# Kernel optimization log

Hardware: AMD Instinct MI355X
Metric: run time of the kernel (lower is better)

Reference implementation:

```python
import jax, jax.numpy as jnp
import numpy as np

N = 40000
E = 640000
IN_FEATS = 128
OUT_FEATS = 64
K = 8
FACTOR_DIM = OUT_FEATS // K  # 8
ITERATIONS = 3
TAU = 1.0
LEAKY_SLOPE = 0.01  # torch nn.LeakyReLU default


def setup_inputs() -> dict:
    key = jax.random.key(0)
    k1, k2, k3 = jax.random.split(key, 3)
    x = jax.random.normal(k1, (N, IN_FEATS), dtype=jnp.float32)
    # xavier_normal_ with gain=1.414: std = gain * sqrt(2 / (fan_in + fan_out))
    std = 1.414 * np.sqrt(2.0 / (IN_FEATS + OUT_FEATS))
    weight = jax.random.normal(k2, (IN_FEATS, OUT_FEATS), dtype=jnp.float32) * std
    bias = jnp.zeros((OUT_FEATS,), dtype=jnp.float32)
    edge_index = jax.random.randint(k3, (2, E), 0, N, dtype=jnp.int32)
    return {"x": x, "weight": weight, "bias": bias, "edge_index": edge_index}


def _l2norm(h):
    # h / ||h||_2 along last dim (no eps, matching torch code)
    return h / jnp.sqrt((h * h).sum(-1, keepdims=True))


def reference(x, weight, bias, edge_index):
    num_nodes = x.shape[0]
    src = edge_index[0]  # scatter target / softmax segment node
    dst = edge_index[1]  # gathered neighbor node

    h = jax.nn.leaky_relu(x @ weight + bias, LEAKY_SLOPE)          # [N, out]
    # split into K factors of FACTOR_DIM: [N, K, d]
    h = h.reshape(num_nodes, K, FACTOR_DIM)
    h_normed = _l2norm(h)                                           # [N, K, d]

    h_src = h_normed
    h_dst = h_normed
    for _ in range(ITERATIONS):
        feat_nbr = h_src[dst]                                       # [E, K, d]
        s = (h_dst[src] * feat_nbr).sum(-1) / TAU                   # [E, K]
        # segment softmax over edges grouped by src node
        smax = jax.ops.segment_max(s, src, num_segments=num_nodes)  # [N, K]
        ex = jnp.exp(s - smax[src])                                 # [E, K]
        denom = jax.ops.segment_sum(ex, src, num_segments=num_nodes)
        alpha = ex / denom[src]                                     # [E, K]
        msg = feat_nbr * alpha[..., None]                           # [E, K, d]
        node_attr = jax.ops.segment_sum(msg, src, num_segments=num_nodes)
        node_attr = node_attr + h_normed                            # [N, K, d]
        h_dst = _l2norm(node_attr)
    return h_dst.reshape(num_nodes, -1)                             # [N, out]
```

## Files before the change

### kernel.cpp

```cpp
#include <hip/hip_runtime.h>
#include <math.h>

#define NN   40000
#define EE   640000
#define INF_ 128
#define OUTF 64
#define SLOTS 64

#define NB32  1250
#define NCOLS 40
#define NBINS (NB32 * NCOLS)
#define SCANA_BLOCKS ((NBINS + 255) / 256)
#define NG4  (EE / 4)

typedef float f2 __attribute__((ext_vector_type(2)));

__device__ __forceinline__ f2 pkfma(f2 a, f2 b, f2 c) {
    return __builtin_elementwise_fma(a, b, c);
}
__device__ __forceinline__ f2 shf2(f2 a, int m) {
    f2 b; b.x = __shfl_xor(a.x, m); b.y = __shfl_xor(a.y, m); return b;
}
__device__ __forceinline__ f2 bfpair(unsigned u) {
    f2 c;
    c.x = __uint_as_float(u << 16);
    c.y = __uint_as_float(u & 0xffff0000u);
    return c;
}
__device__ __forceinline__ unsigned short f2bf(float f) {
    unsigned u = __float_as_uint(f);
    return (unsigned short)((u + 0x7fffu + ((u >> 16) & 1u)) >> 16);
}


__global__ __launch_bounds__(256) void count_gemm_k(
        const float* __restrict__ x, const float* __restrict__ w,
        const float* __restrict__ bias, float* __restrict__ hn,
        unsigned short* __restrict__ hn16,
        const int4* __restrict__ src4, int* __restrict__ binsT,
        uchar4* __restrict__ lrank4) {
    __shared__ float wl[INF_ * OUTF];
    __shared__ float xl[4][8 * 132];

    if (blockIdx.x < NCOLS) {
        int b = blockIdx.x;
        int* lbin = (int*)wl;
        for (int i = threadIdx.x; i < NB32; i += 256) lbin[i] = 0;
        __syncthreads();
#pragma unroll
        for (int rnd = 0; rnd < 16; ++rnd) {
            int gi = b * 4096 + rnd * 256 + threadIdx.x;
            if (gi < NG4) {
                int4 s = src4[gi];
                uchar4 lr;
                lr.x = (unsigned char)atomicAdd(&lbin[s.x >> 5], 1);
                lr.y = (unsigned char)atomicAdd(&lbin[s.y >> 5], 1);
                lr.z = (unsigned char)atomicAdd(&lbin[s.z >> 5], 1);
                lr.w = (unsigned char)atomicAdd(&lbin[s.w >> 5], 1);
                lrank4[gi] = lr;
            }
        }
        __syncthreads();
        for (int u = threadIdx.x; u < NB32; u += 256) binsT[u * NCOLS + b] = lbin[u];
        return;
    }

    for (int i = threadIdx.x; i < INF_ * OUTF; i += 256) wl[i] = w[i];

    int wv = threadIdx.x >> 6;
    int l  = threadIdx.x & 63;
    int q  = l >> 4;
    int rr = l & 15;
    float4 bv = ((const float4*)bias)[rr];
    int srow = l >> 5;
    int scol = (l & 31) * 4;

    int nb = ((blockIdx.x - NCOLS) * 4 + wv) * 16;

#pragma unroll
    for (int h = 0; h < 2; ++h) {
        int n0 = nb + h * 8;
        {
            const float4* xs = (const float4*)(x + (size_t)n0 * INF_);
#pragma unroll
            for (int j = 0; j < 4; ++j) {
                float4 v = xs[j * 64 + l];
                *(float4*)&xl[wv][(j * 2 + srow) * 132 + scol] = v;
            }
        }
        if (h == 0) __syncthreads();
        float4 a0 = bv, a1 = bv;
        const float* x0 = &xl[wv][q * 132];
        const float* x1 = &xl[wv][(q + 4) * 132];
#pragma unroll 4
        for (int i = 0; i < INF_; ++i) {
            float4 w4 = ((const float4*)wl)[i * 16 + rr];
            float xv0 = x0[i], xv1 = x1[i];
            a0.x = fmaf(xv0, w4.x, a0.x); a0.y = fmaf(xv0, w4.y, a0.y);
            a0.z = fmaf(xv0, w4.z, a0.z); a0.w = fmaf(xv0, w4.w, a0.w);
            a1.x = fmaf(xv1, w4.x, a1.x); a1.y = fmaf(xv1, w4.y, a1.y);
            a1.z = fmaf(xv1, w4.z, a1.z); a1.w = fmaf(xv1, w4.w, a1.w);
        }
        a0.x = a0.x > 0.f ? a0.x : 0.01f * a0.x;
        a0.y = a0.y > 0.f ? a0.y : 0.01f * a0.y;
        a0.z = a0.z > 0.f ? a0.z : 0.01f * a0.z;
        a0.w = a0.w > 0.f ? a0.w : 0.01f * a0.w;
        a1.x = a1.x > 0.f ? a1.x : 0.01f * a1.x;
        a1.y = a1.y > 0.f ? a1.y : 0.01f * a1.y;
        a1.z = a1.z > 0.f ? a1.z : 0.01f * a1.z;
        a1.w = a1.w > 0.f ? a1.w : 0.01f * a1.w;
        float s0 = a0.x*a0.x + a0.y*a0.y + a0.z*a0.z + a0.w*a0.w;
        float s1 = a1.x*a1.x + a1.y*a1.y + a1.z*a1.z + a1.w*a1.w;
        s0 += __shfl_xor(s0, 1);
        s1 += __shfl_xor(s1, 1);
        float v0 = rsqrtf(s0), v1 = rsqrtf(s1);
        float4 o0 = make_float4(a0.x*v0, a0.y*v0, a0.z*v0, a0.w*v0);
        float4 o1 = make_float4(a1.x*v1, a1.y*v1, a1.z*v1, a1.w*v1);
        ((float4*)hn)[(size_t)(n0 + q) * 16 + rr] = o0;
        ((float4*)hn)[(size_t)(n0 + 4 + q) * 16 + rr] = o1;
        ushort4 u0, u1;
        u0.x = f2bf(o0.x); u0.y = f2bf(o0.y); u0.z = f2bf(o0.z); u0.w = f2bf(o0.w);
        u1.x = f2bf(o1.x); u1.y = f2bf(o1.y); u1.z = f2bf(o1.z); u1.w = f2bf(o1.w);
        ((ushort4*)hn16)[(size_t)(n0 + q) * 16 + rr] = u0;
        ((ushort4*)hn16)[(size_t)(n0 + 4 + q) * 16 + rr] = u1;
    }
}


__global__ void scanA_k(const int* __restrict__ binsT, int* __restrict__ excl,
                        int* __restrict__ bsum) {
    __shared__ int tmp[256];
    int i = blockIdx.x * 256 + threadIdx.x;
    int v = (i < NBINS) ? binsT[i] : 0;
    tmp[threadIdx.x] = v;
    __syncthreads();
    for (int off = 1; off < 256; off <<= 1) {
        int t = (threadIdx.x >= off) ? tmp[threadIdx.x - off] : 0;
        __syncthreads();
        tmp[threadIdx.x] += t;
        __syncthreads();
    }
    if (i < NBINS) excl[i] = tmp[threadIdx.x] - v;
    if (threadIdx.x == 255) bsum[blockIdx.x] = tmp[255];
}

__device__ __forceinline__ void spine_scan(const int* __restrict__ bsum, int* spine) {
    int v = (threadIdx.x < SCANA_BLOCKS) ? bsum[threadIdx.x] : 0;
    spine[threadIdx.x] = v;
    __syncthreads();
    for (int off = 1; off < 256; off <<= 1) {
        int t = (threadIdx.x >= off) ? spine[threadIdx.x - off] : 0;
        __syncthreads();
        spine[threadIdx.x] += t;
        __syncthreads();
    }
    spine[threadIdx.x] -= v;
    __syncthreads();
}


__global__ __launch_bounds__(256) void part_k(const int4* __restrict__ src4,
                                              const int4* __restrict__ dst4,
                                              const uchar4* __restrict__ lrank4,
                                              const int* __restrict__ excl,
                                              const int* __restrict__ bsum,
                                              unsigned* __restrict__ part) {
    __shared__ int spine[256];
    spine_scan(bsum, spine);

    int gi = blockIdx.x * 256 + threadIdx.x;
    int b  = gi >> 12;
    int4 s = src4[gi];
    int4 d = dst4[gi];
    uchar4 lr = lrank4[gi];
    int i0 = (s.x >> 5) * NCOLS + b;
    int i1 = (s.y >> 5) * NCOLS + b;
    int i2 = (s.z >> 5) * NCOLS + b;
    int i3 = (s.w >> 5) * NCOLS + b;
    part[excl[i0] + spine[i0 >> 8] + lr.x] = ((unsigned)d.x << 5) | (unsigned)(s.x & 31);
    part[excl[i1] + spine[i1 >> 8] + lr.y] = ((unsigned)d.y << 5) | (unsigned)(s.y & 31);
    part[excl[i2] + spine[i2 >> 8] + lr.z] = ((unsigned)d.z << 5) | (unsigned)(s.z & 31);
    part[excl[i3] + spine[i3 >> 8] + lr.w] = ((unsigned)d.w << 5) | (unsigned)(s.w & 31);
}


__global__ __launch_bounds__(256) void attn_build_k(const uint4* __restrict__ hg,
                                                    const float* __restrict__ hnf,
                                                    float* __restrict__ out,
                                                    const unsigned* __restrict__ part,
                                                    const int* __restrict__ excl,
                                                    const int* __restrict__ bsum) {
    __shared__ unsigned short csr_l[32][SLOTS];
    __shared__ int cnt[32];
    __shared__ int spine[256];

    spine_scan(bsum, spine);

    int nb = blockIdx.x;
    if (threadIdx.x < 32) cnt[threadIdx.x] = 0;
    __syncthreads();

    int iu = nb * NCOLS;
    int beg = excl[iu] + spine[iu >> 8];
    int end = EE;
    if (nb + 1 < NB32) {
        int iv = (nb + 1) * NCOLS;
        end = excl[iv] + spine[iv >> 8];
    }
    for (int e = beg + threadIdx.x; e < end; e += 256) {
        unsigned p = part[e];
        int lo = (int)(p & 31u);
        int lr = atomicAdd(&cnt[lo], 1);
        if (lr < SLOTS) csr_l[lo][lr] = (unsigned short)(p >> 5);
    }
    __syncthreads();

    int wv = threadIdx.x >> 6;
    int l  = threadIdx.x & 63;
    int pp_ = l >> 5, q = (l >> 3) & 3, r = l & 7;
    int nbase = nb * 32;

#pragma unroll 1
    for (int pass = 0; pass < 4; ++pass) {
        int ln = pass * 8 + wv * 2 + pp_;
        int n  = nbase + ln;
        if (n >= NN) continue;

        const unsigned short* row = csr_l[ln];
        int deg = min(cnt[ln], SLOTS);

        bool k0 = q      < deg;
        bool k1 = q + 4  < deg;
        bool k2 = q + 8  < deg;
        bool k3 = q + 12 < deg;
        bool k4 = q + 16 < deg;
        bool k5 = q + 20 < deg;
        bool k6 = q + 24 < deg;
        bool k7 = q + 28 < deg;
        unsigned i0 = min((unsigned)row[q     ], NN - 1u);
        unsigned i1 = min((unsigned)row[q +  4], NN - 1u);
        unsigned i2 = min((unsigned)row[q +  8], NN - 1u);
        unsigned i3 = min((unsigned)row[q + 12], NN - 1u);
        unsigned i4 = min((unsigned)row[q + 16], NN - 1u);
        unsigned i5 = min((unsigned)row[q + 20], NN - 1u);
        unsigned i6 = min((unsigned)row[q + 24], NN - 1u);
        unsigned i7 = min((unsigned)row[q + 28], NN - 1u);
        uint4 g0 = hg[(size_t)i0 * 8 + r];
        uint4 g1 = hg[(size_t)i1 * 8 + r];
        uint4 g2 = hg[(size_t)i2 * 8 + r];
        uint4 g3 = hg[(size_t)i3 * 8 + r];
        uint4 g4 = hg[(size_t)i4 * 8 + r];
        uint4 g5 = hg[(size_t)i5 * 8 + r];
        uint4 g6 = hg[(size_t)i6 * 8 + r];
        uint4 g7 = hg[(size_t)i7 * 8 + r];

        f2 e0c0 = bfpair(g0.x), e0c1 = bfpair(g0.y), e0c2 = bfpair(g0.z), e0c3 = bfpair(g0.w);
        f2 e1c0 = bfpair(g1.x), e1c1 = bfpair(g1.y), e1c2 = bfpair(g1.z), e1c3 = bfpair(g1.w);
        f2 e2c0 = bfpair(g2.x), e2c1 = bfpair(g2.y), e2c2 = bfpair(g2.z), e2c3 = bfpair(g2.w);
        f2 e3c0 = bfpair(g3.x), e3c1 = bfpair(g3.y), e3c2 = bfpair(g3.z), e3c3 = bfpair(g3.w);
        f2 e4c0 = bfpair(g4.x), e4c1 = bfpair(g4.y), e4c2 = bfpair(g4.z), e4c3 = bfpair(g4.w);
        f2 e5c0 = bfpair(g5.x), e5c1 = bfpair(g5.y), e5c2 = bfpair(g5.z), e5c3 = bfpair(g5.w);
        f2 e6c0 = bfpair(g6.x), e6c1 = bfpair(g6.y), e6c2 = bfpair(g6.z), e6c3 = bfpair(g6.w);
        f2 e7c0 = bfpair(g7.x), e7c1 = bfpair(g7.y), e7c2 = bfpair(g7.z), e7c3 = bfpair(g7.w);

        const float4* hs4 = (const float4*)(hnf + (size_t)n * OUTF + r * 8);
        float4 ha = hs4[0], hb = hs4[1];
        f2 hs01 = {ha.x, ha.y}, hs23 = {ha.z, ha.w};
        f2 hs45 = {hb.x, hb.y}, hs67 = {hb.z, hb.w};
        f2 hd01 = hs01, hd23 = hs23, hd45 = hs45, hd67 = hs67;

        for (int it = 0; it < 3; ++it) {
            float ssum = 0.f;
            f2 A0 = {0.f, 0.f}, A1 = A0, A2 = A0, A3 = A0;

            auto proc = [&](f2 c0, f2 c1, f2 c2, f2 c3, bool ok) {
                f2 d = c0 * hd01;
                d = pkfma(c1, hd23, d);
                d = pkfma(c2, hd45, d);
                d = pkfma(c3, hd67, d);
                float dd = d.x + d.y;
                float ex = ok ? __expf(dd) : 0.f;
                ssum += ex;
                f2 exv = {ex, ex};
                A0 = pkfma(c0, exv, A0);
                A1 = pkfma(c1, exv, A1);
                A2 = pkfma(c2, exv, A2);
                A3 = pkfma(c3, exv, A3);
            };

            proc(e0c0, e0c1, e0c2, e0c3, k0);
            proc(e1c0, e1c1, e1c2, e1c3, k1);
            proc(e2c0, e2c1, e2c2, e2c3, k2);
            proc(e3c0, e3c1, e3c2, e3c3, k3);
            proc(e4c0, e4c1, e4c2, e4c3, k4);
            proc(e5c0, e5c1, e5c2, e5c3, k5);
            proc(e6c0, e6c1, e6c2, e6c3, k6);
            proc(e7c0, e7c1, e7c2, e7c3, k7);

            for (int e = 32 + q; e < deg; e += 4) {
                unsigned ii = min((unsigned)row[e], NN - 1u);
                uint4 g = hg[(size_t)ii * 8 + r];
                proc(bfpair(g.x), bfpair(g.y), bfpair(g.z), bfpair(g.w), true);
            }

#pragma unroll
            for (int m = 8; m < 32; m <<= 1) {
                ssum += __shfl_xor(ssum, m);
                A0 += shf2(A0, m);
                A1 += shf2(A1, m);
                A2 += shf2(A2, m);
                A3 += shf2(A3, m);
            }

            float rs = (ssum > 0.f) ? 1.f / ssum : 0.f;
            f2 rsv = {rs, rs};
            f2 t01 = pkfma(A0, rsv, hs01);
            f2 t23 = pkfma(A1, rsv, hs23);
            f2 t45 = pkfma(A2, rsv, hs45);
            f2 t67 = pkfma(A3, rsv, hs67);
            f2 d = t01 * t01;
            d = pkfma(t23, t23, d);
            d = pkfma(t45, t45, d);
            d = pkfma(t67, t67, d);
            float inv = rsqrtf(d.x + d.y);
            f2 iv = {inv, inv};
            hd01 = t01 * iv; hd23 = t23 * iv; hd45 = t45 * iv; hd67 = t67 * iv;
        }

        if (q == 0) {
            float4* o4 = (float4*)(out + (size_t)n * OUTF + r * 8);
            o4[0] = make_float4(hd01.x, hd01.y, hd23.x, hd23.y);
            o4[1] = make_float4(hd45.x, hd45.y, hd67.x, hd67.y);
        }
    }
}


extern "C" void kernel_launch(void* const* d_in, const int* in_sizes, int n_in,
                              void* d_out, int out_size, void* d_ws, size_t ws_size,
                              hipStream_t stream) {
    const float* x    = (const float*)d_in[0];
    const float* w    = (const float*)d_in[1];
    const float* bias = (const float*)d_in[2];
    const int*   ei   = (const int*)d_in[3];
    const int*   src  = ei;
    const int*   dst  = ei + EE;
    float* out = (float*)d_out;

    char* ws = (char*)d_ws;
    size_t off = 0;
    float*          hn    = (float*)(ws + off);          off += (size_t)NN * OUTF * 4;
    unsigned short* hn16  = (unsigned short*)(ws + off); off += (size_t)NN * OUTF * 2;
    int*            binsT = (int*)(ws + off);            off += (size_t)NBINS * 4 + 16;
    int*            excl  = (int*)(ws + off);            off += (size_t)NBINS * 4 + 16;
    int*            bsum  = (int*)(ws + off);            off += 1024;
    uchar4*         lrank = (uchar4*)(ws + off);         off += (size_t)EE;
    unsigned*       part  = (unsigned*)(ws + off);       off += (size_t)EE * 4;
    (void)ws_size; (void)in_sizes; (void)n_in; (void)out_size;

    count_gemm_k<<<NCOLS + 625, 256, 0, stream>>>(
        x, w, bias, hn, hn16, (const int4*)src, binsT, lrank);

    scanA_k<<<SCANA_BLOCKS, 256, 0, stream>>>(binsT, excl, bsum);

    part_k<<<NG4 / 256, 256, 0, stream>>>((const int4*)src, (const int4*)dst,
                                          (const uchar4*)lrank, excl, bsum, part);

    attn_build_k<<<NB32, 256, 0, stream>>>((const uint4*)hn16, hn, out,
                                           part, excl, bsum);
}
```

Baseline: 66.15 us.

## Split attention blocks into quarters, drop fp32 hn, restructure GEMM to stream x

```diff
diff --git a/kernel.cpp b/kernel.cpp
--- a/kernel.cpp
+++ b/kernel.cpp
@@ -31,16 +31,34 @@
     unsigned u = __float_as_uint(f);
     return (unsigned short)((u + 0x7fffu + ((u >> 16) & 1u)) >> 16);
 }
+__device__ __forceinline__ float4 f4ma(float s, float4 w, float4 a) {
+    a.x = fmaf(s, w.x, a.x); a.y = fmaf(s, w.y, a.y);
+    a.z = fmaf(s, w.z, a.z); a.w = fmaf(s, w.w, a.w);
+    return a;
+}
+
+__device__ __forceinline__ void spine_scan(const int* __restrict__ bsum, int* spine) {
+    int v = (threadIdx.x < SCANA_BLOCKS) ? bsum[threadIdx.x] : 0;
+    spine[threadIdx.x] = v;
+    __syncthreads();
+    for (int off = 1; off < 256; off <<= 1) {
+        int t = (threadIdx.x >= off) ? spine[threadIdx.x - off] : 0;
+        __syncthreads();
+        spine[threadIdx.x] += t;
+        __syncthreads();
+    }
+    spine[threadIdx.x] -= v;
+    __syncthreads();
+}
 
 
 __global__ __launch_bounds__(256) void count_gemm_k(
         const float* __restrict__ x, const float* __restrict__ w,
-        const float* __restrict__ bias, float* __restrict__ hn,
+        const float* __restrict__ bias,
         unsigned short* __restrict__ hn16,
         const int4* __restrict__ src4, int* __restrict__ binsT,
         uchar4* __restrict__ lrank4) {
     __shared__ float wl[INF_ * OUTF];
-    __shared__ float xl[4][8 * 132];
 
     if (blockIdx.x < NCOLS) {
         int b = blockIdx.x;
@@ -66,63 +84,54 @@
     }
 
     for (int i = threadIdx.x; i < INF_ * OUTF; i += 256) wl[i] = w[i];
+    __syncthreads();
 
     int wv = threadIdx.x >> 6;
     int l  = threadIdx.x & 63;
     int q  = l >> 4;
     int rr = l & 15;
     float4 bv = ((const float4*)bias)[rr];
-    int srow = l >> 5;
-    int scol = (l & 31) * 4;
 
     int nb = ((blockIdx.x - NCOLS) * 4 + wv) * 16;
-
+    const float4* x0 = (const float4*)(x + (size_t)(nb + q     ) * INF_);
+    const float4* x1 = (const float4*)(x + (size_t)(nb + q + 4 ) * INF_);
+    const float4* x2 = (const float4*)(x + (size_t)(nb + q + 8 ) * INF_);
+    const float4* x3 = (const float4*)(x + (size_t)(nb + q + 12) * INF_);
+
+    float4 a0 = bv, a1 = bv, a2 = bv, a3 = bv;
+#pragma unroll 2
+    for (int i4 = 0; i4 < INF_ / 4; ++i4) {
+        float4 v0 = x0[i4];
+        float4 v1 = x1[i4];
+        float4 v2 = x2[i4];
+        float4 v3 = x3[i4];
+        const float4* wp = ((const float4*)wl) + (i4 * 4) * 16 + rr;
+        float4 w0 = wp[0], w1 = wp[16], w2 = wp[32], w3 = wp[48];
+        a0 = f4ma(v0.x, w0, a0); a0 = f4ma(v0.y, w1, a0);
+        a0 = f4ma(v0.z, w2, a0); a0 = f4ma(v0.w, w3, a0);
+        a1 = f4ma(v1.x, w0, a1); a1 = f4ma(v1.y, w1, a1);
+        a1 = f4ma(v1.z, w2, a1); a1 = f4ma(v1.w, w3, a1);
+        a2 = f4ma(v2.x, w0, a2); a2 = f4ma(v2.y, w1, a2);
+        a2 = f4ma(v2.z, w2, a2); a2 = f4ma(v2.w, w3, a2);
+        a3 = f4ma(v3.x, w0, a3); a3 = f4ma(v3.y, w1, a3);
+        a3 = f4ma(v3.z, w2, a3); a3 = f4ma(v3.w, w3, a3);
+    }
+
+    float4 acc[4] = {a0, a1, a2, a3};
 #pragma unroll
-    for (int h = 0; h < 2; ++h) {
-        int n0 = nb + h * 8;
-        {
-            const float4* xs = (const float4*)(x + (size_t)n0 * INF_);
-#pragma unroll
-            for (int j = 0; j < 4; ++j) {
-                float4 v = xs[j * 64 + l];
-                *(float4*)&xl[wv][(j * 2 + srow) * 132 + scol] = v;
-            }
-        }
-        if (h == 0) __syncthreads();
-        float4 a0 = bv, a1 = bv;
-        const float* x0 = &xl[wv][q * 132];
-        const float* x1 = &xl[wv][(q + 4) * 132];
-#pragma unroll 4
-        for (int i = 0; i < INF_; ++i) {
-            float4 w4 = ((const float4*)wl)[i * 16 + rr];
-            float xv0 = x0[i], xv1 = x1[i];
-            a0.x = fmaf(xv0, w4.x, a0.x); a0.y = fmaf(xv0, w4.y, a0.y);
-            a0.z = fmaf(xv0, w4.z, a0.z); a0.w = fmaf(xv0, w4.w, a0.w);
-            a1.x = fmaf(xv1, w4.x, a1.x); a1.y = fmaf(xv1, w4.y, a1.y);
-            a1.z = fmaf(xv1, w4.z, a1.z); a1.w = fmaf(xv1, w4.w, a1.w);
-        }
-        a0.x = a0.x > 0.f ? a0.x : 0.01f * a0.x;
-        a0.y = a0.y > 0.f ? a0.y : 0.01f * a0.y;
-        a0.z = a0.z > 0.f ? a0.z : 0.01f * a0.z;
-        a0.w = a0.w > 0.f ? a0.w : 0.01f * a0.w;
-        a1.x = a1.x > 0.f ? a1.x : 0.01f * a1.x;
-        a1.y = a1.y > 0.f ? a1.y : 0.01f * a1.y;
-        a1.z = a1.z > 0.f ? a1.z : 0.01f * a1.z;
-        a1.w = a1.w > 0.f ? a1.w : 0.01f * a1.w;
-        float s0 = a0.x*a0.x + a0.y*a0.y + a0.z*a0.z + a0.w*a0.w;
-        float s1 = a1.x*a1.x + a1.y*a1.y + a1.z*a1.z + a1.w*a1.w;
-        s0 += __shfl_xor(s0, 1);
-        s1 += __shfl_xor(s1, 1);
-        float v0 = rsqrtf(s0), v1 = rsqrtf(s1);
-        float4 o0 = make_float4(a0.x*v0, a0.y*v0, a0.z*v0, a0.w*v0);
-        float4 o1 = make_float4(a1.x*v1, a1.y*v1, a1.z*v1, a1.w*v1);
-        ((float4*)hn)[(size_t)(n0 + q) * 16 + rr] = o0;
-        ((float4*)hn)[(size_t)(n0 + 4 + q) * 16 + rr] = o1;
-        ushort4 u0, u1;
-        u0.x = f2bf(o0.x); u0.y = f2bf(o0.y); u0.z = f2bf(o0.z); u0.w = f2bf(o0.w);
-        u1.x = f2bf(o1.x); u1.y = f2bf(o1.y); u1.z = f2bf(o1.z); u1.w = f2bf(o1.w);
-        ((ushort4*)hn16)[(size_t)(n0 + q) * 16 + rr] = u0;
-        ((ushort4*)hn16)[(size_t)(n0 + 4 + q) * 16 + rr] = u1;
+    for (int k = 0; k < 4; ++k) {
+        float4 a = acc[k];
+        a.x = a.x > 0.f ? a.x : 0.01f * a.x;
+        a.y = a.y > 0.f ? a.y : 0.01f * a.y;
+        a.z = a.z > 0.f ? a.z : 0.01f * a.z;
+        a.w = a.w > 0.f ? a.w : 0.01f * a.w;
+        float sq = a.x*a.x + a.y*a.y + a.z*a.z + a.w*a.w;
+        sq += __shfl_xor(sq, 1);
+        float inv = rsqrtf(sq);
+        ushort4 u;
+        u.x = f2bf(a.x*inv); u.y = f2bf(a.y*inv);
+        u.z = f2bf(a.z*inv); u.w = f2bf(a.w*inv);
+        ((ushort4*)hn16)[(size_t)(nb + q + 4*k) * 16 + rr] = u;
     }
 }
 
@@ -142,20 +151,6 @@
     }
     if (i < NBINS) excl[i] = tmp[threadIdx.x] - v;
     if (threadIdx.x == 255) bsum[blockIdx.x] = tmp[255];
-}
-
-__device__ __forceinline__ void spine_scan(const int* __restrict__ bsum, int* spine) {
-    int v = (threadIdx.x < SCANA_BLOCKS) ? bsum[threadIdx.x] : 0;
-    spine[threadIdx.x] = v;
-    __syncthreads();
-    for (int off = 1; off < 256; off <<= 1) {
-        int t = (threadIdx.x >= off) ? spine[threadIdx.x - off] : 0;
-        __syncthreads();
-        spine[threadIdx.x] += t;
-        __syncthreads();
-    }
-    spine[threadIdx.x] -= v;
-    __syncthreads();
 }
 
 
@@ -185,153 +180,150 @@
 
 
 __global__ __launch_bounds__(256) void attn_build_k(const uint4* __restrict__ hg,
-                                                    const float* __restrict__ hnf,
                                                     float* __restrict__ out,
                                                     const unsigned* __restrict__ part,
                                                     const int* __restrict__ excl,
                                                     const int* __restrict__ bsum) {
-    __shared__ unsigned short csr_l[32][SLOTS];
-    __shared__ int cnt[32];
+    __shared__ unsigned short csr_l[8][SLOTS];
+    __shared__ int cnt8[8];
     __shared__ int spine[256];
 
     spine_scan(bsum, spine);
 
-    int nb = blockIdx.x;
-    if (threadIdx.x < 32) cnt[threadIdx.x] = 0;
-    __syncthreads();
-
-    int iu = nb * NCOLS;
+    int g = blockIdx.x;
+    int u = g >> 2;
+    int c = g & 3;
+    if (threadIdx.x < 8) cnt8[threadIdx.x] = 0;
+    __syncthreads();
+
+    int iu = u * NCOLS;
     int beg = excl[iu] + spine[iu >> 8];
     int end = EE;
-    if (nb + 1 < NB32) {
-        int iv = (nb + 1) * NCOLS;
+    if (u + 1 < NB32) {
+        int iv = (u + 1) * NCOLS;
         end = excl[iv] + spine[iv >> 8];
     }
     for (int e = beg + threadIdx.x; e < end; e += 256) {
         unsigned p = part[e];
         int lo = (int)(p & 31u);
-        int lr = atomicAdd(&cnt[lo], 1);
-        if (lr < SLOTS) csr_l[lo][lr] = (unsigned short)(p >> 5);
+        if ((lo >> 3) == c) {
+            int ll = lo & 7;
+            int lr = atomicAdd(&cnt8[ll], 1);
+            if (lr < SLOTS) csr_l[ll][lr] = (unsigned short)(p >> 5);
+        }
     }
     __syncthreads();
 
     int wv = threadIdx.x >> 6;
     int l  = threadIdx.x & 63;
     int pp_ = l >> 5, q = (l >> 3) & 3, r = l & 7;
-    int nbase = nb * 32;
-
-#pragma unroll 1
-    for (int pass = 0; pass < 4; ++pass) {
-        int ln = pass * 8 + wv * 2 + pp_;
-        int n  = nbase + ln;
-        if (n >= NN) continue;
-
-        const unsigned short* row = csr_l[ln];
-        int deg = min(cnt[ln], SLOTS);
-
-        bool k0 = q      < deg;
-        bool k1 = q + 4  < deg;
-        bool k2 = q + 8  < deg;
-        bool k3 = q + 12 < deg;
-        bool k4 = q + 16 < deg;
-        bool k5 = q + 20 < deg;
-        bool k6 = q + 24 < deg;
-        bool k7 = q + 28 < deg;
-        unsigned i0 = min((unsigned)row[q     ], NN - 1u);
-        unsigned i1 = min((unsigned)row[q +  4], NN - 1u);
-        unsigned i2 = min((unsigned)row[q +  8], NN - 1u);
-        unsigned i3 = min((unsigned)row[q + 12], NN - 1u);
-        unsigned i4 = min((unsigned)row[q + 16], NN - 1u);
-        unsigned i5 = min((unsigned)row[q + 20], NN - 1u);
-        unsigned i6 = min((unsigned)row[q + 24], NN - 1u);
-        unsigned i7 = min((unsigned)row[q + 28], NN - 1u);
-        uint4 g0 = hg[(size_t)i0 * 8 + r];
-        uint4 g1 = hg[(size_t)i1 * 8 + r];
-        uint4 g2 = hg[(size_t)i2 * 8 + r];
-        uint4 g3 = hg[(size_t)i3 * 8 + r];
-        uint4 g4 = hg[(size_t)i4 * 8 + r];
-        uint4 g5 = hg[(size_t)i5 * 8 + r];
-        uint4 g6 = hg[(size_t)i6 * 8 + r];
-        uint4 g7 = hg[(size_t)i7 * 8 + r];
-
-        f2 e0c0 = bfpair(g0.x), e0c1 = bfpair(g0.y), e0c2 = bfpair(g0.z), e0c3 = bfpair(g0.w);
-        f2 e1c0 = bfpair(g1.x), e1c1 = bfpair(g1.y), e1c2 = bfpair(g1.z), e1c3 = bfpair(g1.w);
-        f2 e2c0 = bfpair(g2.x), e2c1 = bfpair(g2.y), e2c2 = bfpair(g2.z), e2c3 = bfpair(g2.w);
-        f2 e3c0 = bfpair(g3.x), e3c1 = bfpair(g3.y), e3c2 = bfpair(g3.z), e3c3 = bfpair(g3.w);
-        f2 e4c0 = bfpair(g4.x), e4c1 = bfpair(g4.y), e4c2 = bfpair(g4.z), e4c3 = bfpair(g4.w);
-        f2 e5c0 = bfpair(g5.x), e5c1 = bfpair(g5.y), e5c2 = bfpair(g5.z), e5c3 = bfpair(g5.w);
-        f2 e6c0 = bfpair(g6.x), e6c1 = bfpair(g6.y), e6c2 = bfpair(g6.z), e6c3 = bfpair(g6.w);
-        f2 e7c0 = bfpair(g7.x), e7c1 = bfpair(g7.y), e7c2 = bfpair(g7.z), e7c3 = bfpair(g7.w);
-
-        const float4* hs4 = (const float4*)(hnf + (size_t)n * OUTF + r * 8);
-        float4 ha = hs4[0], hb = hs4[1];
-        f2 hs01 = {ha.x, ha.y}, hs23 = {ha.z, ha.w};
-        f2 hs45 = {hb.x, hb.y}, hs67 = {hb.z, hb.w};
-        f2 hd01 = hs01, hd23 = hs23, hd45 = hs45, hd67 = hs67;
-
-        for (int it = 0; it < 3; ++it) {
-            float ssum = 0.f;
-            f2 A0 = {0.f, 0.f}, A1 = A0, A2 = A0, A3 = A0;
-
-            auto proc = [&](f2 c0, f2 c1, f2 c2, f2 c3, bool ok) {
-                f2 d = c0 * hd01;
-                d = pkfma(c1, hd23, d);
-                d = pkfma(c2, hd45, d);
-                d = pkfma(c3, hd67, d);
-                float dd = d.x + d.y;
-                float ex = ok ? __expf(dd) : 0.f;
-                ssum += ex;
-                f2 exv = {ex, ex};
-                A0 = pkfma(c0, exv, A0);
-                A1 = pkfma(c1, exv, A1);
-                A2 = pkfma(c2, exv, A2);
-                A3 = pkfma(c3, exv, A3);
-            };
-
-            proc(e0c0, e0c1, e0c2, e0c3, k0);
-            proc(e1c0, e1c1, e1c2, e1c3, k1);
-            proc(e2c0, e2c1, e2c2, e2c3, k2);
-            proc(e3c0, e3c1, e3c2, e3c3, k3);
-            proc(e4c0, e4c1, e4c2, e4c3, k4);
-            proc(e5c0, e5c1, e5c2, e5c3, k5);
-            proc(e6c0, e6c1, e6c2, e6c3, k6);
-            proc(e7c0, e7c1, e7c2, e7c3, k7);
-
-            for (int e = 32 + q; e < deg; e += 4) {
-                unsigned ii = min((unsigned)row[e], NN - 1u);
-                uint4 g = hg[(size_t)ii * 8 + r];
-                proc(bfpair(g.x), bfpair(g.y), bfpair(g.z), bfpair(g.w), true);
-            }
+    int ln = wv * 2 + pp_;
+    int n  = u * 32 + c * 8 + ln;
+
+    const unsigned short* row = csr_l[ln];
+    int deg = min(cnt8[ln], SLOTS);
+
+    bool k0 = q      < deg;
+    bool k1 = q + 4  < deg;
+    bool k2 = q + 8  < deg;
+    bool k3 = q + 12 < deg;
+    bool k4 = q + 16 < deg;
+    bool k5 = q + 20 < deg;
+    bool k6 = q + 24 < deg;
+    bool k7 = q + 28 < deg;
+    unsigned i0 = min((unsigned)row[q     ], NN - 1u);
+    unsigned i1 = min((unsigned)row[q +  4], NN - 1u);
+    unsigned i2 = min((unsigned)row[q +  8], NN - 1u);
+    unsigned i3 = min((unsigned)row[q + 12], NN - 1u);
+    unsigned i4 = min((unsigned)row[q + 16], NN - 1u);
+    unsigned i5 = min((unsigned)row[q + 20], NN - 1u);
+    unsigned i6 = min((unsigned)row[q + 24], NN - 1u);
+    unsigned i7 = min((unsigned)row[q + 28], NN - 1u);
+    uint4 g0 = hg[(size_t)i0 * 8 + r];
+    uint4 g1 = hg[(size_t)i1 * 8 + r];
+    uint4 g2 = hg[(size_t)i2 * 8 + r];
+    uint4 g3 = hg[(size_t)i3 * 8 + r];
+    uint4 g4 = hg[(size_t)i4 * 8 + r];
+    uint4 g5 = hg[(size_t)i5 * 8 + r];
+    uint4 g6 = hg[(size_t)i6 * 8 + r];
+    uint4 g7 = hg[(size_t)i7 * 8 + r];
+    uint4 hself = hg[(size_t)n * 8 + r];
+
+    f2 e0c0 = bfpair(g0.x), e0c1 = bfpair(g0.y), e0c2 = bfpair(g0.z), e0c3 = bfpair(g0.w);
+    f2 e1c0 = bfpair(g1.x), e1c1 = bfpair(g1.y), e1c2 = bfpair(g1.z), e1c3 = bfpair(g1.w);
+    f2 e2c0 = bfpair(g2.x), e2c1 = bfpair(g2.y), e2c2 = bfpair(g2.z), e2c3 = bfpair(g2.w);
+    f2 e3c0 = bfpair(g3.x), e3c1 = bfpair(g3.y), e3c2 = bfpair(g3.z), e3c3 = bfpair(g3.w);
+    f2 e4c0 = bfpair(g4.x), e4c1 = bfpair(g4.y), e4c2 = bfpair(g4.z), e4c3 = bfpair(g4.w);
+    f2 e5c0 = bfpair(g5.x), e5c1 = bfpair(g5.y), e5c2 = bfpair(g5.z), e5c3 = bfpair(g5.w);
+    f2 e6c0 = bfpair(g6.x), e6c1 = bfpair(g6.y), e6c2 = bfpair(g6.z), e6c3 = bfpair(g6.w);
+    f2 e7c0 = bfpair(g7.x), e7c1 = bfpair(g7.y), e7c2 = bfpair(g7.z), e7c3 = bfpair(g7.w);
+
+    f2 hs01 = bfpair(hself.x), hs23 = bfpair(hself.y);
+    f2 hs45 = bfpair(hself.z), hs67 = bfpair(hself.w);
+    f2 hd01 = hs01, hd23 = hs23, hd45 = hs45, hd67 = hs67;
+
+    for (int it = 0; it < 3; ++it) {
+        float ssum = 0.f;
+        f2 A0 = {0.f, 0.f}, A1 = A0, A2 = A0, A3 = A0;
+
+        auto proc = [&](f2 c0, f2 c1, f2 c2, f2 c3, bool ok) {
+            f2 d = c0 * hd01;
+            d = pkfma(c1, hd23, d);
+            d = pkfma(c2, hd45, d);
+            d = pkfma(c3, hd67, d);
+            float dd = d.x + d.y;
+            float ex = ok ? __expf(dd) : 0.f;
+            ssum += ex;
+            f2 exv = {ex, ex};
+            A0 = pkfma(c0, exv, A0);
+            A1 = pkfma(c1, exv, A1);
+            A2 = pkfma(c2, exv, A2);
+            A3 = pkfma(c3, exv, A3);
+        };
+
+        proc(e0c0, e0c1, e0c2, e0c3, k0);
+        proc(e1c0, e1c1, e1c2, e1c3, k1);
+        proc(e2c0, e2c1, e2c2, e2c3, k2);
+        proc(e3c0, e3c1, e3c2, e3c3, k3);
+        proc(e4c0, e4c1, e4c2, e4c3, k4);
+        proc(e5c0, e5c1, e5c2, e5c3, k5);
+        proc(e6c0, e6c1, e6c2, e6c3, k6);
+        proc(e7c0, e7c1, e7c2, e7c3, k7);
+
+        for (int e = 32 + q; e < deg; e += 4) {
+            unsigned ii = min((unsigned)row[e], NN - 1u);
+            uint4 gg = hg[(size_t)ii * 8 + r];
+            proc(bfpair(gg.x), bfpair(gg.y), bfpair(gg.z), bfpair(gg.w), true);
+        }
 
 #pragma unroll
-            for (int m = 8; m < 32; m <<= 1) {
-                ssum += __shfl_xor(ssum, m);
-                A0 += shf2(A0, m);
-                A1 += shf2(A1, m);
-                A2 += shf2(A2, m);
-                A3 += shf2(A3, m);
-            }
-
-            float rs = (ssum > 0.f) ? 1.f / ssum : 0.f;
-            f2 rsv = {rs, rs};
-            f2 t01 = pkfma(A0, rsv, hs01);
-            f2 t23 = pkfma(A1, rsv, hs23);
-            f2 t45 = pkfma(A2, rsv, hs45);
-            f2 t67 = pkfma(A3, rsv, hs67);
-            f2 d = t01 * t01;
-            d = pkfma(t23, t23, d);
-            d = pkfma(t45, t45, d);
-            d = pkfma(t67, t67, d);
-            float inv = rsqrtf(d.x + d.y);
-            f2 iv = {inv, inv};
-            hd01 = t01 * iv; hd23 = t23 * iv; hd45 = t45 * iv; hd67 = t67 * iv;
+        for (int m = 8; m < 32; m <<= 1) {
+            ssum += __shfl_xor(ssum, m);
+            A0 += shf2(A0, m);
+            A1 += shf2(A1, m);
+            A2 += shf2(A2, m);
+            A3 += shf2(A3, m);
         }
 
-        if (q == 0) {
-            float4* o4 = (float4*)(out + (size_t)n * OUTF + r * 8);
-            o4[0] = make_float4(hd01.x, hd01.y, hd23.x, hd23.y);
-            o4[1] = make_float4(hd45.x, hd45.y, hd67.x, hd67.y);
-        }
+        float rs = (ssum > 0.f) ? 1.f / ssum : 0.f;
+        f2 rsv = {rs, rs};
+        f2 t01 = pkfma(A0, rsv, hs01);
+        f2 t23 = pkfma(A1, rsv, hs23);
+        f2 t45 = pkfma(A2, rsv, hs45);
+        f2 t67 = pkfma(A3, rsv, hs67);
+        f2 d = t01 * t01;
+        d = pkfma(t23, t23, d);
+        d = pkfma(t45, t45, d);
+        d = pkfma(t67, t67, d);
+        float inv = rsqrtf(d.x + d.y);
+        f2 iv = {inv, inv};
+        hd01 = t01 * iv; hd23 = t23 * iv; hd45 = t45 * iv; hd67 = t67 * iv;
+    }
+
+    if (q == 0) {
+        float4* o4 = (float4*)(out + (size_t)n * OUTF + r * 8);
+        o4[0] = make_float4(hd01.x, hd01.y, hd23.x, hd23.y);
+        o4[1] = make_float4(hd45.x, hd45.y, hd67.x, hd67.y);
     }
 }
 
@@ -349,7 +341,6 @@
 
     char* ws = (char*)d_ws;
     size_t off = 0;
-    float*          hn    = (float*)(ws + off);          off += (size_t)NN * OUTF * 4;
     unsigned short* hn16  = (unsigned short*)(ws + off); off += (size_t)NN * OUTF * 2;
     int*            binsT = (int*)(ws + off);            off += (size_t)NBINS * 4 + 16;
     int*            excl  = (int*)(ws + off);            off += (size_t)NBINS * 4 + 16;
@@ -359,13 +350,13 @@
     (void)ws_size; (void)in_sizes; (void)n_in; (void)out_size;
 
     count_gemm_k<<<NCOLS + 625, 256, 0, stream>>>(
-        x, w, bias, hn, hn16, (const int4*)src, binsT, lrank);
+        x, w, bias, hn16, (const int4*)src, binsT, lrank);
 
     scanA_k<<<SCANA_BLOCKS, 256, 0, stream>>>(binsT, excl, bsum);
 
     part_k<<<NG4 / 256, 256, 0, stream>>>((const int4*)src, (const int4*)dst,
                                           (const uchar4*)lrank, excl, bsum, part);
 
-    attn_build_k<<<NB32, 256, 0, stream>>>((const uint4*)hn16, hn, out,
-                                           part, excl, bsum);
-}
+    attn_build_k<<<NB32 * 4, 256, 0, stream>>>((const uint4*)hn16, out,
+                                               part, excl, bsum);
+}
```

After: 70.45 us. +6.5%, slower.
